# Kernel optimization log

Measured on AMD Instinct MI355X. Metric: run time of the kernel, lower is better.

## Reference

```python
import jax, jax.numpy as jnp
import numpy as np

B = 65536       # batch of (head, tail) triples
S = 512         # num_neg_samples
D = 100         # embed_size
HV = 100000     # head entity vocab
TV = 188047     # tail entity vocab (hard-coded 188047 in original)


def setup_inputs() -> dict:
    key = jax.random.key(0)
    k1, k2, k3, k4, k5, k6 = jax.random.split(key, 6)
    initrange = 0.5 / D
    head_table = jax.random.uniform(k1, (HV + 1, D), minval=-initrange, maxval=initrange, dtype=jnp.float32)
    tail_table = jax.random.uniform(k2, (TV + 1, D), minval=-initrange, maxval=initrange, dtype=jnp.float32)
    rel_vec = jax.random.uniform(k3, (1, D), minval=-initrange, maxval=initrange, dtype=jnp.float32)
    rel_bias = jnp.zeros((TV + 1,), dtype=jnp.float32)  # original inits bias to zeros
    head_idx = jax.random.randint(k4, (B,), 0, HV)
    tail_idx = jax.random.randint(k5, (B,), 0, TV)
    # stands in for torch.multinomial(distrib, num_samples, replacement=True)
    neg_idx = jax.random.randint(k6, (S,), 0, TV)
    return dict(head_table=head_table, tail_table=tail_table, rel_vec=rel_vec,
                rel_bias=rel_bias, head_idx=head_idx, tail_idx=tail_idx, neg_idx=neg_idx)


def reference(head_table, tail_table, rel_vec, rel_bias, head_idx, tail_idx, neg_idx):
    # entity_head_vec = entity_head_embed(idxs); example_vec = head + relation
    h = head_table[head_idx]                      # [B, D]
    ex = h + rel_vec                              # [B, D]
    t = tail_table[tail_idx]                      # [B, D]
    bias = rel_bias[tail_idx]                     # [B]
    # pos_logits = bmm(pos_vec, example_vec) + relation_bias
    pos_logits = jnp.einsum('bd,bd->b', t, ex) + bias
    pos_loss = -jax.nn.log_sigmoid(pos_logits)    # = -log(sigmoid(x)), stable
    # shared negatives: neg_logits = example_vec @ neg_vec.T + bias
    neg = tail_table[neg_idx]                     # [S, D]
    neg_logits = ex @ neg.T + bias[:, None]       # [B, S]
    neg_loss = -jax.nn.log_sigmoid(-neg_logits).sum(axis=1)
    return jnp.mean(pos_loss + neg_loss)
```

## Files before the change

kernel.cpp:

```cpp
#include <hip/hip_runtime.h>
#include <stdint.h>

typedef __attribute__((ext_vector_type(4))) float   f4;
typedef __attribute__((ext_vector_type(8))) short   short8;
typedef __attribute__((ext_vector_type(4))) float   floatx4;
typedef __attribute__((ext_vector_type(4))) unsigned int u32x4;

#define LN2F 0.6931471805599453f

#define BB 65536
#define SS 512
#define DD 100

__device__ __forceinline__ unsigned short f2bf(float f) {
  union { float f; unsigned int u; } v; v.f = f;
  unsigned int u = v.u;
  u += 0x7fffu + ((u >> 16) & 1u);
  return (unsigned short)(u >> 16);
}
__device__ __forceinline__ u32x4 pack8(f4 a, f4 b) {
  u32x4 r;
  r.x = (unsigned int)f2bf(a[0]) | ((unsigned int)f2bf(a[1]) << 16);
  r.y = (unsigned int)f2bf(a[2]) | ((unsigned int)f2bf(a[3]) << 16);
  r.z = (unsigned int)f2bf(b[0]) | ((unsigned int)f2bf(b[1]) << 16);
  r.w = (unsigned int)f2bf(b[2]) | ((unsigned int)f2bf(b[3]) << 16);
  return r;
}
__device__ __forceinline__ float softplus_full(float x) {
  return fmaxf(x, 0.f) + log1pf(expf(-fabsf(x)));
}

__global__ __launch_bounds__(256) void negprep_k(
    const float* __restrict__ tail_table, const int* __restrict__ neg_idx,
    u32x4* __restrict__ nws, float* __restrict__ out) {
  if (blockIdx.x == 0 && threadIdx.x == 0) out[0] = 0.f;
  int tid = blockIdx.x * 256 + threadIdx.x;
  int s = tid >> 4, kg = tid & 15, k0 = kg * 8;
  int nrow = neg_idx[s];
  const float* np = tail_table + (size_t)nrow * DD;
  const int aoff = (kg <= 12) ? k0     : 0;
  const int boff = (kg <  12) ? k0 + 4 : 4;
  f4 a = *(const f4*)(np + aoff);
  f4 b = *(const f4*)(np + boff);
  if (kg > 12)  a = (f4){0.f,0.f,0.f,0.f};
  if (kg >= 12) b = (f4){0.f,0.f,0.f,0.f};
  nws[((s >> 4) * 4 + (kg >> 2)) * 64 + (s & 15) + 16 * (kg & 3)] = pack8(a, b);
}

__global__ __launch_bounds__(256, 4) void keg_main(
    const float* __restrict__ head_table, const float* __restrict__ tail_table,
    const float* __restrict__ rel_vec,   const float* __restrict__ rel_bias,
    const int* __restrict__ head_idx,    const int* __restrict__ tail_idx,
    const u32x4* __restrict__ nws,       float* __restrict__ out) {
  __shared__ u32x4 exA4[1024];
  __shared__ __align__(16) float bias_s[64];
  __shared__ float red[4];

  const int t = threadIdx.x;
  const int kg = t & 15, rid = t >> 4, k0 = kg * 8;
  const int bbase = blockIdx.x * 64;

  f4 ra = {0,0,0,0}, rb = {0,0,0,0};
  if (kg <= 12) ra = *(const f4*)(rel_vec + k0);
  if (kg <  12) rb = *(const f4*)(rel_vec + k0 + 4);

  const int aoff = (kg <= 12) ? k0     : 0;
  const int boff = (kg <  12) ? k0 + 4 : 4;

  const float* hp[4]; const float* tp[4];
  float biasv[4];
  #pragma unroll
  for (int p = 0; p < 4; ++p) {
    int R = bbase + p * 16 + rid;
    hp[p] = head_table + (size_t)head_idx[R] * DD;
    int trow = tail_idx[R];
    tp[p] = tail_table + (size_t)trow * DD;
    biasv[p] = rel_bias[trow];
  }
  f4 ha[4], hb[4], ta[4], tb[4];
  #pragma unroll
  for (int p = 0; p < 4; ++p) {
    ha[p] = *(const f4*)(hp[p] + aoff);
    hb[p] = *(const f4*)(hp[p] + boff);
    ta[p] = *(const f4*)(tp[p] + aoff);
    tb[p] = *(const f4*)(tp[p] + boff);
  }

  float pos_acc = 0.f;
  #pragma unroll
  for (int p = 0; p < 4; ++p) {
    f4 e0 = ha[p] + ra, e1 = hb[p] + rb;
    if (kg > 12)  e0 = (f4){0.f,0.f,0.f,0.f};
    if (kg >= 12) e1 = (f4){0.f,0.f,0.f,0.f};
    exA4[(p * 4 + (kg >> 2)) * 64 + rid + 16 * (kg & 3)] = pack8(e0, e1);
    float d = e0[0]*ta[p][0] + e0[1]*ta[p][1] + e0[2]*ta[p][2] + e0[3]*ta[p][3]
            + e1[0]*tb[p][0] + e1[1]*tb[p][1] + e1[2]*tb[p][2] + e1[3]*tb[p][3];
    d += __shfl_xor(d, 1); d += __shfl_xor(d, 2);
    d += __shfl_xor(d, 4); d += __shfl_xor(d, 8);
    if (kg == 0) {
      bias_s[p * 16 + rid] = biasv[p];
      pos_acc += softplus_full(-(d + biasv[p]));
    }
  }
  __syncthreads();

  const int w = t >> 6, lane = t & 63, quad = lane >> 4;
  const short8* exAs = (const short8*)exA4;
  const short8* nf   = (const short8*)nws;

  short8 afr[4][4];
  #pragma unroll
  for (int mf = 0; mf < 4; ++mf)
    #pragma unroll
    for (int ks = 0; ks < 4; ++ks)
      afr[mf][ks] = exAs[(mf * 4 + ks) * 64 + lane];

  float nacc = 0.f;
  #pragma unroll 2
  for (int g = 0; g < 8; ++g) {
    int ng = w * 8 + g;
    short8 bfr[4];
    #pragma unroll
    for (int ks = 0; ks < 4; ++ks)
      bfr[ks] = nf[(ng * 4 + ks) * 64 + lane];
    floatx4 acc[4];
    #pragma unroll
    for (int mf = 0; mf < 4; ++mf)
      acc[mf] = *(const floatx4*)&bias_s[mf * 16 + quad * 4];
    #pragma unroll
    for (int ks = 0; ks < 4; ++ks)
      #pragma unroll
      for (int mf = 0; mf < 4; ++mf)
        acc[mf] = __builtin_amdgcn_mfma_f32_16x16x32_bf16(afr[mf][ks], bfr[ks], acc[mf], 0, 0, 0);
    float s1 = 0.f, s2 = 0.f, gmax = 0.f;
    #pragma unroll
    for (int mf = 0; mf < 4; ++mf)
      #pragma unroll
      for (int r = 0; r < 4; ++r) {
        float x = acc[mf][r];
        s1 += x;
        s2 = fmaf(x, x, s2);
        gmax = fmaxf(gmax, fabsf(x));
      }
    if (__ballot(gmax < 0.03f) == ~0ULL) {
      nacc += fmaf(s1, 0.5f, fmaf(s2, 0.125f, 16.f * LN2F));
    } else {
      #pragma unroll
      for (int mf = 0; mf < 4; ++mf)
        #pragma unroll
        for (int r = 0; r < 4; ++r)
          nacc += softplus_full(acc[mf][r]);
    }
  }

  float tot = nacc + pos_acc;
  #pragma unroll
  for (int off = 32; off; off >>= 1) tot += __shfl_down(tot, off);
  if (lane == 0) red[w] = tot;
  __syncthreads();
  if (t == 0)
    atomicAdd(out, (red[0] + red[1] + red[2] + red[3]) * (1.0f / (float)BB));
}

extern "C" void kernel_launch(void* const* d_in, const int* in_sizes, int n_in,
                              void* d_out, int out_size, void* d_ws, size_t ws_size,
                              hipStream_t stream) {
  const float* head_table = (const float*)d_in[0];
  const float* tail_table = (const float*)d_in[1];
  const float* rel_vec    = (const float*)d_in[2];
  const float* rel_bias   = (const float*)d_in[3];
  const int*   head_idx   = (const int*)d_in[4];
  const int*   tail_idx   = (const int*)d_in[5];
  const int*   neg_idx    = (const int*)d_in[6];
  float* out = (float*)d_out;

  u32x4* nws = (u32x4*)d_ws;

  negprep_k<<<32, 256, 0, stream>>>(tail_table, neg_idx, nws, out);
  keg_main<<<1024, 256, 0, stream>>>(head_table, tail_table, rel_vec, rel_bias,
                                     head_idx, tail_idx, (const u32x4*)nws, out);
}
```

Baseline: 169.8 us.

## Split block tile into two halves to overlap packing with MFMA

The 64-row example tile is split into two 32-row halves, each with its own LDS buffer and bias slice. Packing and the positive score for half 0 run first, then a light LDS-only barrier, then the MFMA stage for half 0, and only then is half 1 packed and processed. The aim is to let the first half's matrix work start while gathers for the second half are still in flight, and to use the cheaper barrier in place of __syncthreads. The cost is that the negative-sample B fragments are now loaded twice per block, and the Taylor-branch ballot runs on smaller groups.

```diff
diff --git a/kernel.cpp b/kernel.cpp
--- a/kernel.cpp
+++ b/kernel.cpp
@@ -28,6 +28,10 @@
 }
 __device__ __forceinline__ float softplus_full(float x) {
   return fmaxf(x, 0.f) + log1pf(expf(-fabsf(x)));
+}
+__device__ __forceinline__ void lds_barrier() {
+  asm volatile("s_waitcnt lgkmcnt(0)" ::: "memory");
+  __builtin_amdgcn_s_barrier();
 }
 
 __global__ __launch_bounds__(256) void negprep_k(
@@ -47,111 +51,134 @@
   nws[((s >> 4) * 4 + (kg >> 2)) * 64 + (s & 15) + 16 * (kg & 3)] = pack8(a, b);
 }
 
-__global__ __launch_bounds__(256, 4) void keg_main(
+__global__ __launch_bounds__(256, 4) void keg_pipe(
     const float* __restrict__ head_table, const float* __restrict__ tail_table,
     const float* __restrict__ rel_vec,   const float* __restrict__ rel_bias,
     const int* __restrict__ head_idx,    const int* __restrict__ tail_idx,
     const u32x4* __restrict__ nws,       float* __restrict__ out) {
-  __shared__ u32x4 exA4[1024];
-  __shared__ __align__(16) float bias_s[64];
+  __shared__ u32x4 exA4[2][512];
+  __shared__ __align__(16) float bias_s[2][32];
   __shared__ float red[4];
 
   const int t = threadIdx.x;
-  const int kg = t & 15, rid = t >> 4, k0 = kg * 8;
+  const int kg = t & 15, grp = t >> 4, k0 = kg * 8;
   const int bbase = blockIdx.x * 64;
 
   f4 ra = {0,0,0,0}, rb = {0,0,0,0};
   if (kg <= 12) ra = *(const f4*)(rel_vec + k0);
   if (kg <  12) rb = *(const f4*)(rel_vec + k0 + 4);
-
   const int aoff = (kg <= 12) ? k0     : 0;
   const int boff = (kg <  12) ? k0 + 4 : 4;
 
-  const float* hp[4]; const float* tp[4];
-  float biasv[4];
+  const float* hp[2][2]; const float* tp[2][2]; float biasv[2][2];
   #pragma unroll
-  for (int p = 0; p < 4; ++p) {
-    int R = bbase + p * 16 + rid;
-    hp[p] = head_table + (size_t)head_idx[R] * DD;
-    int trow = tail_idx[R];
-    tp[p] = tail_table + (size_t)trow * DD;
-    biasv[p] = rel_bias[trow];
+  for (int T = 0; T < 2; ++T)
+    #pragma unroll
+    for (int p = 0; p < 2; ++p) {
+      int R = bbase + T * 32 + p * 16 + grp;
+      hp[T][p] = head_table + (size_t)head_idx[R] * DD;
+      int trow = tail_idx[R];
+      tp[T][p] = tail_table + (size_t)trow * DD;
+      biasv[T][p] = rel_bias[trow];
+    }
+
+  f4 ha[2][2], hb[2][2], ta[2][2], tb[2][2];
+  #pragma unroll
+  for (int T = 0; T < 2; ++T)
+    #pragma unroll
+    for (int p = 0; p < 2; ++p) {
+      ha[T][p] = *(const f4*)(hp[T][p] + aoff);
+      hb[T][p] = *(const f4*)(hp[T][p] + boff);
+      ta[T][p] = *(const f4*)(tp[T][p] + aoff);
+      tb[T][p] = *(const f4*)(tp[T][p] + boff);
+    }
+
+  const int w = t >> 6, lane = t & 63, quad = lane >> 4;
+  const short8* nf = (const short8*)nws;
+  float pos_acc = 0.f, nacc = 0.f;
+
+#define PACK_TILE(T)                                                          \
+  {                                                                           \
+    _Pragma("unroll")                                                         \
+    for (int p = 0; p < 2; ++p) {                                             \
+      f4 e0 = ha[T][p] + ra, e1 = hb[T][p] + rb;                              \
+      if (kg > 12)  e0 = (f4){0.f,0.f,0.f,0.f};                               \
+      if (kg >= 12) e1 = (f4){0.f,0.f,0.f,0.f};                               \
+      exA4[T][(p * 4 + (kg >> 2)) * 64 + grp + 16 * (kg & 3)] = pack8(e0, e1);\
+      float d = e0[0]*ta[T][p][0] + e0[1]*ta[T][p][1] + e0[2]*ta[T][p][2]     \
+              + e0[3]*ta[T][p][3] + e1[0]*tb[T][p][0] + e1[1]*tb[T][p][1]     \
+              + e1[2]*tb[T][p][2] + e1[3]*tb[T][p][3];                        \
+      d += __shfl_xor(d, 1); d += __shfl_xor(d, 2);                           \
+      d += __shfl_xor(d, 4); d += __shfl_xor(d, 8);                           \
+      if (kg == 0) {                                                          \
+        bias_s[T][p * 16 + grp] = biasv[T][p];                                \
+        pos_acc += softplus_full(-(d + biasv[T][p]));                         \
+      }                                                                       \
+    }                                                                         \
   }
-  f4 ha[4], hb[4], ta[4], tb[4];
-  #pragma unroll
-  for (int p = 0; p < 4; ++p) {
-    ha[p] = *(const f4*)(hp[p] + aoff);
-    hb[p] = *(const f4*)(hp[p] + boff);
-    ta[p] = *(const f4*)(tp[p] + aoff);
-    tb[p] = *(const f4*)(tp[p] + boff);
+
+#define MFMA_STAGE(B)                                                         \
+  {                                                                           \
+    const short8* exAs = (const short8*)exA4[B];                              \
+    short8 afr[2][4];                                                         \
+    float  br[2][4];                                                          \
+    _Pragma("unroll")                                                         \
+    for (int m = 0; m < 2; ++m) {                                             \
+      _Pragma("unroll")                                                       \
+      for (int ks = 0; ks < 4; ++ks) afr[m][ks] = exAs[(m * 4 + ks) * 64 + lane]; \
+      _Pragma("unroll")                                                       \
+      for (int r = 0; r < 4; ++r)   br[m][r]  = bias_s[B][m * 16 + quad * 4 + r]; \
+    }                                                                         \
+    _Pragma("unroll 2")                                                       \
+    for (int g = 0; g < 8; ++g) {                                             \
+      int ng = w * 8 + g;                                                     \
+      short8 bfr[4];                                                          \
+      _Pragma("unroll")                                                       \
+      for (int ks = 0; ks < 4; ++ks)                                          \
+        bfr[ks] = nf[(ng * 4 + ks) * 64 + lane];                  \
+      floatx4 acc[2];                                                         \
+      _Pragma("unroll")                                                       \
+      for (int m = 0; m < 2; ++m) {                   \
+        floatx4 c; c[0]=br[m][0]; c[1]=br[m][1]; c[2]=br[m][2]; c[3]=br[m][3];\
+        acc[m] = c;                                                           \
+      }                                                                       \
+      _Pragma("unroll")                                                       \
+      for (int ks = 0; ks < 4; ++ks)                                          \
+        _Pragma("unroll")                                                     \
+        for (int m = 0; m < 2; ++m)                                           \
+          acc[m] = __builtin_amdgcn_mfma_f32_16x16x32_bf16(afr[m][ks], bfr[ks], acc[m], 0, 0, 0); \
+      float s1 = 0.f, s2 = 0.f, gmax = 0.f;                                   \
+      _Pragma("unroll")                                                       \
+      for (int m = 0; m < 2; ++m)                                             \
+        _Pragma("unroll")                                                     \
+        for (int r = 0; r < 4; ++r) {                                         \
+          float x = acc[m][r];                                                \
+          s1 += x;                                                            \
+          s2 = fmaf(x, x, s2);                                                \
+          gmax = fmaxf(gmax, fabsf(x));                                       \
+        }                                                                     \
+      if (__ballot(gmax < 0.03f) == ~0ULL) {                                  \
+        \
+        nacc += fmaf(s1, 0.5f, fmaf(s2, 0.125f, 8.f * LN2F));                 \
+      } else {                                                                \
+        _Pragma("unroll")                                                     \
+        for (int m = 0; m < 2; ++m)                                           \
+          _Pragma("unroll")                                                   \
+          for (int r = 0; r < 4; ++r)                                         \
+            nacc += softplus_full(acc[m][r]);                                 \
+      }                                                                       \
+    }                                                                         \
   }
 
-  float pos_acc = 0.f;
-  #pragma unroll
-  for (int p = 0; p < 4; ++p) {
-    f4 e0 = ha[p] + ra, e1 = hb[p] + rb;
-    if (kg > 12)  e0 = (f4){0.f,0.f,0.f,0.f};
-    if (kg >= 12) e1 = (f4){0.f,0.f,0.f,0.f};
-    exA4[(p * 4 + (kg >> 2)) * 64 + rid + 16 * (kg & 3)] = pack8(e0, e1);
-    float d = e0[0]*ta[p][0] + e0[1]*ta[p][1] + e0[2]*ta[p][2] + e0[3]*ta[p][3]
-            + e1[0]*tb[p][0] + e1[1]*tb[p][1] + e1[2]*tb[p][2] + e1[3]*tb[p][3];
-    d += __shfl_xor(d, 1); d += __shfl_xor(d, 2);
-    d += __shfl_xor(d, 4); d += __shfl_xor(d, 8);
-    if (kg == 0) {
-      bias_s[p * 16 + rid] = biasv[p];
-      pos_acc += softplus_full(-(d + biasv[p]));
-    }
-  }
-  __syncthreads();
-
-  const int w = t >> 6, lane = t & 63, quad = lane >> 4;
-  const short8* exAs = (const short8*)exA4;
-  const short8* nf   = (const short8*)nws;
-
-  short8 afr[4][4];
-  #pragma unroll
-  for (int mf = 0; mf < 4; ++mf)
-    #pragma unroll
-    for (int ks = 0; ks < 4; ++ks)
-      afr[mf][ks] = exAs[(mf * 4 + ks) * 64 + lane];
-
-  float nacc = 0.f;
-  #pragma unroll 2
-  for (int g = 0; g < 8; ++g) {
-    int ng = w * 8 + g;
-    short8 bfr[4];
-    #pragma unroll
-    for (int ks = 0; ks < 4; ++ks)
-      bfr[ks] = nf[(ng * 4 + ks) * 64 + lane];
-    floatx4 acc[4];
-    #pragma unroll
-    for (int mf = 0; mf < 4; ++mf)
-      acc[mf] = *(const floatx4*)&bias_s[mf * 16 + quad * 4];
-    #pragma unroll
-    for (int ks = 0; ks < 4; ++ks)
-      #pragma unroll
-      for (int mf = 0; mf < 4; ++mf)
-        acc[mf] = __builtin_amdgcn_mfma_f32_16x16x32_bf16(afr[mf][ks], bfr[ks], acc[mf], 0, 0, 0);
-    float s1 = 0.f, s2 = 0.f, gmax = 0.f;
-    #pragma unroll
-    for (int mf = 0; mf < 4; ++mf)
-      #pragma unroll
-      for (int r = 0; r < 4; ++r) {
-        float x = acc[mf][r];
-        s1 += x;
-        s2 = fmaf(x, x, s2);
-        gmax = fmaxf(gmax, fabsf(x));
-      }
-    if (__ballot(gmax < 0.03f) == ~0ULL) {
-      nacc += fmaf(s1, 0.5f, fmaf(s2, 0.125f, 16.f * LN2F));
-    } else {
-      #pragma unroll
-      for (int mf = 0; mf < 4; ++mf)
-        #pragma unroll
-        for (int r = 0; r < 4; ++r)
-          nacc += softplus_full(acc[mf][r]);
-    }
-  }
+  PACK_TILE(0)
+  lds_barrier();
+  MFMA_STAGE(0)
+  PACK_TILE(1)
+  lds_barrier();
+  MFMA_STAGE(1)
+
+#undef PACK_TILE
+#undef MFMA_STAGE
 
   float tot = nacc + pos_acc;
   #pragma unroll
@@ -177,6 +204,6 @@
   u32x4* nws = (u32x4*)d_ws;
 
   negprep_k<<<32, 256, 0, stream>>>(tail_table, neg_idx, nws, out);
-  keg_main<<<1024, 256, 0, stream>>>(head_table, tail_table, rel_vec, rel_bias,
+  keg_pipe<<<1024, 256, 0, stream>>>(head_table, tail_table, rel_vec, rel_bias,
                                      head_idx, tail_idx, (const u32x4*)nws, out);
 }
```

Result: faster. 166.4 us (-2.0%).
